# Optimization experiments

Hardware: AMD Instinct MI355X
Metric: run time of the kernel (lower is better)

The kernel has to match this reference:

```python
import jax, jax.numpy as jnp
import numpy as np

B_ = 2; L_ = 4096; D_MODEL = 1024; D_INNER = 2048; D_STATE = 128
N_HEADS = 32; HEADDIM = 64; D_CONV = 4; CHUNK = 64
CONV_DIM = D_INNER + 2 * D_STATE
EPS = 1e-5


def silu(x):
    return x * jax.nn.sigmoid(x)


def segsum(x):
    # x: (..., T) -> (..., T, T) stable segment sums; exp() gives 1-semiseparable matrix
    T = x.shape[-1]
    xe = jnp.broadcast_to(x[..., None], x.shape + (T,))  # (..., T, T)
    lower = jnp.tril(jnp.ones((T, T), bool), -1)
    xs = jnp.cumsum(jnp.where(lower, xe, 0.0), axis=-2)
    incl = jnp.tril(jnp.ones((T, T), bool), 0)
    return jnp.where(incl, xs, -jnp.inf)


def ssd(x, A, Bm, Cm):
    # x: (b, l, h, p); A: (b, l, h); Bm/Cm: (b, l, n) (single shared head, as in module)
    b, l, h, p = x.shape
    c = l // CHUNK
    x = x.reshape(b, c, CHUNK, h, p)
    A = A.reshape(b, c, CHUNK, h).transpose(0, 3, 1, 2)  # (b, h, c, l)
    Bm = Bm.reshape(b, c, CHUNK, D_STATE)
    Cm = Cm.reshape(b, c, CHUNK, D_STATE)
    A_cumsum = jnp.cumsum(A, axis=-1)                    # (b, h, c, l)
    Lmat = jnp.exp(segsum(A))                            # (b, h, c, l, l)
    # intra-chunk (diagonal blocks)
    Y_diag = jnp.einsum('bcln,bcsn,bhcls,bcshp->bclhp', Cm, Bm, Lmat, x)
    # per-chunk states
    decay_states = jnp.exp(A_cumsum[:, :, :, -1:] - A_cumsum)  # (b, h, c, l)
    states = jnp.einsum('bcln,bhcl,bclhp->bchpn', Bm, decay_states, x)
    init = jnp.zeros_like(states[:, :1])
    states = jnp.concatenate([init, states], axis=1)     # (b, c+1, h, p, n)
    A_last = jnp.pad(A_cumsum[:, :, :, -1], ((0, 0), (0, 0), (1, 0)))  # (b, h, c+1)
    decay_chunk = jnp.exp(segsum(A_last))                # (b, h, c+1, c+1)
    new_states = jnp.einsum('bhzc,bchpn->bzhpn', decay_chunk, states)
    states_prev = new_states[:, :-1]                     # (b, c, h, p, n)
    state_decay_out = jnp.exp(A_cumsum)
    Y_off = jnp.einsum('bcln,bchpn,bhcl->bclhp', Cm, states_prev, state_decay_out)
    return (Y_diag + Y_off).reshape(b, l, h, p)


def setup_inputs() -> dict:
    key = jax.random.key(0)
    ks = jax.random.split(key, 9)
    u = jax.random.normal(ks[0], (B_, L_, D_MODEL), jnp.float32)
    W_in = jax.random.normal(ks[1], (2 * D_INNER + 2 * D_STATE + N_HEADS, D_MODEL), jnp.float32) * (D_MODEL ** -0.5)
    conv_w = jax.random.normal(ks[2], (CONV_DIM, 1, D_CONV), jnp.float32) * 0.2
    conv_b = jax.random.normal(ks[3], (CONV_DIM,), jnp.float32) * 0.02
    dt_bias = jax.random.normal(ks[4], (N_HEADS,), jnp.float32) * 0.1
    A_log = jnp.log(jax.random.uniform(ks[5], (N_HEADS,), jnp.float32, 1.0, 16.0))
    D_param = jax.random.normal(ks[6], (N_HEADS,), jnp.float32) * 0.5
    norm_w = jnp.ones((D_INNER,), jnp.float32)
    W_out = jax.random.normal(ks[7], (D_MODEL, D_INNER), jnp.float32) * (D_INNER ** -0.5)
    return dict(u=u, W_in=W_in, conv_w=conv_w, conv_b=conv_b, dt_bias=dt_bias,
                A_log=A_log, D_param=D_param, norm_w=norm_w, W_out=W_out)


def mamba_forward(u, W_in, conv_w, conv_b, dt_bias, A_log, D_param, norm_w, W_out):
    b, l, _ = u.shape
    zxbcdt = u @ W_in.T                                  # (b, l, 2*di+2*ds+h)
    z = zxbcdt[..., :D_INNER]
    xBC = zxbcdt[..., D_INNER:D_INNER + CONV_DIM]
    dt = zxbcdt[..., D_INNER + CONV_DIM:]
    dt = jax.nn.softplus(dt + dt_bias)                   # (b, l, h)
    # causal depthwise conv1d
    xc = jnp.transpose(xBC, (0, 2, 1))                   # (b, conv_dim, l)
    xc = jax.lax.conv_general_dilated(xc, conv_w, (1,), [(D_CONV - 1, 0)],
                                      feature_group_count=CONV_DIM,
                                      dimension_numbers=('NCH', 'OIH', 'NCH'))
    xc = xc + conv_b[None, :, None]
    xBC = silu(jnp.transpose(xc, (0, 2, 1)))             # (b, l, conv_dim)
    x = xBC[..., :D_INNER]
    Bc = xBC[..., D_INNER:D_INNER + D_STATE]
    Cc = xBC[..., D_INNER + D_STATE:]
    x = x.reshape(b, l, N_HEADS, HEADDIM)
    A = -jnp.exp(A_log)                                  # (h,)
    Y = ssd(x * dt[..., None], A * dt, Bc, Cc)           # (b, l, h, p)
    y = Y + x * D_param[:, None]
    y = y.reshape(b, l, D_INNER)
    # gated RMSNorm
    y = y * silu(z)
    y = y * jax.lax.rsqrt(jnp.mean(y * y, axis=-1, keepdims=True) + EPS) * norm_w
    return y @ W_out.T


def reference(u, W_in, conv_w, conv_b, dt_bias, A_log, D_param, norm_w, W_out):
    return mamba_forward(u, W_in, conv_w, conv_b, dt_bias, A_log, D_param, norm_w, W_out)
```

## Files before the change

### kernel.cpp

```cpp
#include <hip/hip_runtime.h>
#include <hip/hip_bf16.h>
#include <math.h>

#define B_    2
#define L_    4096
#define DM    1024
#define DI    2048
#define DS    128
#define NH    32
#define HD    64
#define CHUNK 64
#define NC    (L_/CHUNK)
#define CD    (DI + 2*DS)
#define ROWS  (B_*L_)
#define NOUT  (2*DI + 2*DS + NH)
#define NPAD2 4608

typedef __attribute__((ext_vector_type(4))) float f32x4;
typedef __attribute__((ext_vector_type(8))) __bf16 bf16x8;
typedef __attribute__((ext_vector_type(4))) short s16x4;
typedef __attribute__((ext_vector_type(8))) short s16x8;

__global__ __launch_bounds__(256) void k_convert_all(const float* __restrict__ u, const float* __restrict__ W_in,
                                                     const float* __restrict__ W_out, __bf16* __restrict__ ubf,
                                                     __bf16* __restrict__ wibf, __bf16* __restrict__ wobf) {
    int i = blockIdx.x * 256 + threadIdx.x;
    const int QU  = ROWS * DM / 4;
    const int QWI = NPAD2 * DM / 4;
    const int QWO = DM * DI / 4;
    const float* s = nullptr;
    __bf16* d;
    bool zero = false;
    if (i < QU) {
        s = u + (size_t)i * 4; d = ubf + (size_t)i * 4;
    } else if (i < QU + QWI) {
        int j = i - QU;
        d = wibf + (size_t)j * 4;
        if (j < NOUT * DM / 4) s = W_in + (size_t)j * 4; else zero = true;
    } else if (i < QU + QWI + QWO) {
        int j = i - QU - QWI;
        s = W_out + (size_t)j * 4; d = wobf + (size_t)j * 4;
    } else return;
    s16x4 o = {0, 0, 0, 0};
    if (!zero) {
        f32x4 v = *(const f32x4*)s;
#pragma unroll
        for (int q = 0; q < 4; q++) o[q] = __builtin_bit_cast(short, (__bf16)v[q]);
    }
    *(s16x4*)d = o;
}

__device__ __forceinline__ void stage_half(const __bf16* __restrict__ G, int ldg, int grow0, int kt,
                                           char* lds, int ldsoff, int tid, int wave) {
#pragma unroll
    for (int issue = 0; issue < 2; issue++) {
        int o   = issue * 8192 + tid * 16;
        int row = o >> 7;
        int cb  = (o & 127) ^ ((row & 7) << 4);
        const __bf16* src = G + (size_t)(grow0 + row) * ldg + kt + (cb >> 1);
        char* ldsbase = lds + ldsoff + issue * 8192 + wave * 1024;
        __builtin_amdgcn_global_load_lds((const __attribute__((address_space(1))) void*)src,
                                         (__attribute__((address_space(3))) void*)ldsbase,
                                         16, 0, 0);
    }
}

__device__ __forceinline__ bf16x8 rdfrag(const char* lds, int ldsoff, int r, int ks, int lane) {
    int logical = r * 128 + ks * 64 + ((lane >> 4) << 4);
    int phys    = logical ^ ((r & 7) << 4);
    return *(const bf16x8*)(lds + ldsoff + phys);
}

__device__ __forceinline__ void gemm128x128_core(const __bf16* __restrict__ Ag, const __bf16* __restrict__ Bg,
                                                 int K, int m0, int n0, char* lds, f32x4 acc[4][2]) {
    const int tid = threadIdx.x, wave = tid >> 6, lane = tid & 63;
    const int wm = wave >> 2, wn = wave & 3, lrow = lane & 15;
    const int KT = K >> 6;

    for (int t = 0; t < KT; t++) {
        const int kt = t << 6;
        stage_half(Ag, K, m0, kt, lds, 0,     tid, wave);
        stage_half(Bg, K, n0, kt, lds, 16384, tid, wave);
        asm volatile("s_waitcnt vmcnt(0)" ::: "memory");
        __builtin_amdgcn_s_barrier();
        bf16x8 a[4][2];
#pragma unroll
        for (int fm = 0; fm < 4; fm++)
#pragma unroll
            for (int ks = 0; ks < 2; ks++)
                a[fm][ks] = rdfrag(lds, 0, wm * 64 + fm * 16 + lrow, ks, lane);
        __builtin_amdgcn_s_setprio(1);
#pragma unroll
        for (int fn = 0; fn < 2; fn++) {
            bf16x8 b0 = rdfrag(lds, 16384, wn * 32 + fn * 16 + lrow, 0, lane);
            bf16x8 b1 = rdfrag(lds, 16384, wn * 32 + fn * 16 + lrow, 1, lane);
#pragma unroll
            for (int fm = 0; fm < 4; fm++) {
                acc[fm][fn] = __builtin_amdgcn_mfma_f32_16x16x32_bf16(a[fm][0], b0, acc[fm][fn], 0, 0, 0);
                acc[fm][fn] = __builtin_amdgcn_mfma_f32_16x16x32_bf16(a[fm][1], b1, acc[fm][fn], 0, 0, 0);
            }
        }
        __builtin_amdgcn_s_setprio(0);
        __builtin_amdgcn_s_barrier();
    }
}

__global__ __launch_bounds__(512, 4) void k_gemm1(const __bf16* __restrict__ ubf, const __bf16* __restrict__ wibf,
                                                  __bf16* __restrict__ zbuf, __bf16* __restrict__ xbcraw,
                                                  float* __restrict__ dtbuf, const float* __restrict__ dt_bias) {
    extern __shared__ char lds[];
    f32x4 acc[4][2];
    f32x4 z4 = {0.f, 0.f, 0.f, 0.f};
#pragma unroll
    for (int i = 0; i < 4; i++)
#pragma unroll
        for (int j = 0; j < 2; j++) acc[i][j] = z4;

    int bid = blockIdx.x;
    int wg  = (bid & 7) * 280 + (bid >> 3);
    int m0  = (wg / 35) * 128;
    int n0  = (wg % 35) * 128;
    gemm128x128_core(ubf, wibf, DM, m0, n0, lds, acc);

    const int lane = threadIdx.x & 63, wave = threadIdx.x >> 6;
    const int wm = wave >> 2, wn = wave & 3;
    const int gm_base = m0 + wm * 64 + ((lane >> 4) << 2);
    const int gn_base = n0 + wn * 32 + (lane & 15);
#pragma unroll
    for (int fm = 0; fm < 4; fm++) {
        const int gmb = gm_base + fm * 16;
#pragma unroll
        for (int fn = 0; fn < 2; fn++) {
            const int gn = gn_base + fn * 16;
            if (gn < DI) {
#pragma unroll
                for (int r = 0; r < 4; r++)
                    zbuf[(size_t)(gmb + r) * DI + gn] = (__bf16)acc[fm][fn][r];
            } else if (gn < DI + CD) {
#pragma unroll
                for (int r = 0; r < 4; r++)
                    xbcraw[(size_t)(gmb + r) * CD + (gn - DI)] = (__bf16)acc[fm][fn][r];
            } else if (gn < NOUT) {
                const int hh = gn - (DI + CD);
                const float bb = dt_bias[hh];
#pragma unroll
                for (int r = 0; r < 4; r++) {
                    float x = acc[fm][fn][r] + bb;
                    float sp = (x > 20.f) ? x : log1pf(__expf(x));
                    dtbuf[(size_t)(gmb + r) * NH + hh] = sp;
                }
            }
        }
    }
}

__global__ __launch_bounds__(512, 4) void k_gemm2(const __bf16* __restrict__ ybf, const __bf16* __restrict__ wobf,
                                                  float* __restrict__ out) {
    extern __shared__ char lds[];
    f32x4 acc[4][2];
    f32x4 z4 = {0.f, 0.f, 0.f, 0.f};
#pragma unroll
    for (int i = 0; i < 4; i++)
#pragma unroll
        for (int j = 0; j < 2; j++) acc[i][j] = z4;

    int bid = blockIdx.x;
    int wg  = (bid & 7) * 64 + (bid >> 3);
    int m0  = (wg / 8) * 128;
    int n0  = (wg % 8) * 128;
    gemm128x128_core(ybf, wobf, DI, m0, n0, lds, acc);

    const int lane = threadIdx.x & 63, wave = threadIdx.x >> 6;
    const int wm = wave >> 2, wn = wave & 3;
    const int gm_base = m0 + wm * 64 + ((lane >> 4) << 2);
    const int gn_base = n0 + wn * 32 + (lane & 15);
#pragma unroll
    for (int fm = 0; fm < 4; fm++) {
        const int gmb = gm_base + fm * 16;
#pragma unroll
        for (int fn = 0; fn < 2; fn++) {
            const int gn = gn_base + fn * 16;
#pragma unroll
            for (int r = 0; r < 4; r++)
                out[(size_t)(gmb + r) * DM + gn] = acc[fm][fn][r];
        }
    }
}

__global__ __launch_bounds__(256) void k_conv(const __bf16* __restrict__ xbcraw, const float* __restrict__ conv_w,
                                              const float* __restrict__ conv_b, __bf16* __restrict__ xconv) {
    __shared__ float wsh[256 * 4];
    __shared__ float bsh[256];
    const int tid  = threadIdx.x;
    const int gsub = tid & 31;
    const int roct = tid >> 5;
    const int ch_base_blk = blockIdx.x * 256;
    *(f32x4*)&wsh[tid * 4] = *(const f32x4*)&conv_w[ch_base_blk * 4 + tid * 4];
    bsh[tid] = conv_b[ch_base_blk + tid];
    __syncthreads();

    const int ch0  = ch_base_blk + gsub * 8;
    const int row0 = (blockIdx.y * 8 + roct) * 8;
    const int l0   = row0 & (L_ - 1);
    const __bf16* src = xbcraw + (size_t)row0 * CD + ch0;

    s16x8 rr[11];
#pragma unroll
    for (int j = 0; j < 11; j++) {
        int ll = l0 - 3 + j;
        if (ll >= 0) rr[j] = *(const s16x8*)(src + (size_t)(j - 3) * CD);
        else         rr[j] = (s16x8){0, 0, 0, 0, 0, 0, 0, 0};
    }

    const int chl = gsub * 8;
    float w[8][4], bias[8];
#pragma unroll
    for (int j = 0; j < 8; j++) {
        bias[j] = bsh[chl + j];
#pragma unroll
        for (int k = 0; k < 4; k++) w[j][k] = wsh[(chl + j) * 4 + k];
    }

    __bf16* dst = xconv + (size_t)row0 * CD + ch0;
#pragma unroll
    for (int orow = 0; orow < 8; orow++) {
        float a[8];
#pragma unroll
        for (int j = 0; j < 8; j++) a[j] = bias[j];
#pragma unroll
        for (int k = 0; k < 4; k++) {
            s16x8 v = rr[orow + k];
#pragma unroll
            for (int j = 0; j < 8; j++)
                a[j] += w[j][k] * (float)__builtin_bit_cast(__bf16, (short)v[j]);
        }
        s16x8 o;
#pragma unroll
        for (int j = 0; j < 8; j++)
            o[j] = __builtin_bit_cast(short, (__bf16)(a[j] * __builtin_amdgcn_rcpf(1.f + __expf(-a[j]))));
        *(s16x8*)(dst + (size_t)orow * CD) = o;
    }
}

__global__ __launch_bounds__(256) void k_cbt(const __bf16* __restrict__ xconv, float* __restrict__ cbt) {
    const int c = blockIdx.x, b = blockIdx.y;
    const int tid = threadIdx.x, wv = tid >> 6, lane = tid & 63;
    const int lrow = lane & 15, lko = (lane >> 4) * 8;
    __shared__ __align__(16) __bf16 Csh[64 * 136];
    __shared__ __align__(16) __bf16 Bsh[64 * 136];
    const size_t rowbase = (size_t)b * L_ + c * CHUNK;
#pragma unroll
    for (int q = 0; q < 32; q++) {
        int i = q * 2 + (wv >> 1);
        int n = (wv & 1) * 64 + lane;
        const __bf16* base = xconv + (rowbase + i) * CD + DI;
        Bsh[i * 136 + n] = base[n];
        Csh[i * 136 + n] = base[DS + n];
    }
    __syncthreads();
    f32x4 acc[4];
    f32x4 z4 = {0.f, 0.f, 0.f, 0.f};
#pragma unroll
    for (int jt = 0; jt < 4; jt++) acc[jt] = z4;
#pragma unroll
    for (int ks = 0; ks < 4; ks++) {
        bf16x8 a = *(const bf16x8*)&Csh[(wv * 16 + lrow) * 136 + ks * 32 + lko];
#pragma unroll
        for (int jt = 0; jt < 4; jt++) {
            bf16x8 bb = *(const bf16x8*)&Bsh[(jt * 16 + lrow) * 136 + ks * 32 + lko];
            acc[jt] = __builtin_amdgcn_mfma_f32_16x16x32_bf16(a, bb, acc[jt], 0, 0, 0);
        }
    }
    float* o = cbt + (size_t)(b * NC + c) * 4096;
#pragma unroll
    for (int jt = 0; jt < 4; jt++)
#pragma unroll
        for (int r = 0; r < 4; r++) {
            int i = wv * 16 + (lane >> 4) * 4 + r;
            int j = jt * 16 + lrow;
            o[i * 64 + j] = acc[jt][r];
        }
}

__global__ __launch_bounds__(256) void k_ssd_a(const __bf16* __restrict__ xconv, const float* __restrict__ dtbuf,
                                               const float* __restrict__ cbt, const float* __restrict__ A_log,
                                               __bf16* __restrict__ ybuf, __bf16* __restrict__ states,
                                               float* __restrict__ asum, const float* __restrict__ D_param) {
    const int h = blockIdx.x, c = blockIdx.y, b = blockIdx.z;
    const int tid = threadIdx.x, wv = tid >> 6, lane = tid & 63;
    const int lrow = lane & 15, lko = (lane >> 4) * 8;
    __shared__ __align__(16) __bf16 xT[64 * 72];
    __shared__ __align__(16) __bf16 xsc[64 * 72];
    __shared__ __align__(16) __bf16 BT[128 * 72];
    __shared__ __align__(16) __bf16 Ms[64 * 72];
    __shared__ float dts[64], cum[64];

    const float Ah = -__expf(A_log[h]);
    const size_t rowbase = (size_t)b * L_ + c * CHUNK;

    float dtv = 0.f;
    if (wv == 0) { dtv = dtbuf[(rowbase + lane) * NH + h]; dts[lane] = dtv; }
#pragma unroll
    for (int q = 0; q < 16; q++) {
        int i = q * 4 + wv;
        xT[lane * 72 + i] = xconv[(rowbase + i) * CD + h * HD + lane];
    }
#pragma unroll
    for (int q = 0; q < 32; q++) {
        int i = q * 2 + (wv >> 1);
        int n = (wv & 1) * 64 + lane;
        BT[n * 72 + i] = xconv[(rowbase + i) * CD + DI + n];
    }
    if (wv == 0) {
        float v = Ah * dtv;
#pragma unroll
        for (int o = 1; o < 64; o <<= 1) { float t = __shfl_up(v, o); if (lane >= o) v += t; }
        cum[lane] = v;
        if (lane == 63) asum[(b * NC + c) * NH + h] = v;
    }
    __syncthreads();

    const float cum63 = cum[63];
    const float Dh = D_param[h];
    const float* cbt_bc = cbt + (size_t)(b * NC + c) * 4096;
#pragma unroll
    for (int q = 0; q < 16; q++) {
        int i = q * 4 + wv, j = lane;
        float cumi = cum[i];
        float m = 0.f;
        if (j <= i) m = cbt_bc[i * 64 + j] * __expf(cumi - cum[j]) * dts[j];
        if (j == i) m += Dh;
        Ms[i * 72 + j] = (__bf16)m;
        float dcfi = __expf(cum63 - cumi) * dts[i];
        xsc[lane * 72 + i] = (__bf16)((float)xT[lane * 72 + i] * dcfi);
    }
    __syncthreads();

    f32x4 z4 = {0.f, 0.f, 0.f, 0.f};
    {
        f32x4 accY[4];
#pragma unroll
        for (int pt = 0; pt < 4; pt++) accY[pt] = z4;
#pragma unroll
        for (int ks = 0; ks < 2; ks++) {
            bf16x8 a = *(const bf16x8*)&Ms[(wv * 16 + lrow) * 72 + ks * 32 + lko];
#pragma unroll
            for (int pt = 0; pt < 4; pt++) {
                bf16x8 bb = *(const bf16x8*)&xT[(pt * 16 + lrow) * 72 + ks * 32 + lko];
                accY[pt] = __builtin_amdgcn_mfma_f32_16x16x32_bf16(a, bb, accY[pt], 0, 0, 0);
            }
        }
#pragma unroll
        for (int pt = 0; pt < 4; pt++)
#pragma unroll
            for (int r = 0; r < 4; r++) {
                int i = wv * 16 + (lane >> 4) * 4 + r;
                int p = pt * 16 + lrow;
                ybuf[(rowbase + i) * DI + h * HD + p] = (__bf16)accY[pt][r];
            }
    }
    {
        f32x4 accS[8];
#pragma unroll
        for (int nt = 0; nt < 8; nt++) accS[nt] = z4;
#pragma unroll
        for (int ks = 0; ks < 2; ks++) {
            bf16x8 a = *(const bf16x8*)&xsc[(wv * 16 + lrow) * 72 + ks * 32 + lko];
#pragma unroll
            for (int nt = 0; nt < 8; nt++) {
                bf16x8 bb = *(const bf16x8*)&BT[(nt * 16 + lrow) * 72 + ks * 32 + lko];
                accS[nt] = __builtin_amdgcn_mfma_f32_16x16x32_bf16(a, bb, accS[nt], 0, 0, 0);
            }
        }
        __bf16* sp = states + ((size_t)(b * NC + c) * NH + h) * 8192;
#pragma unroll
        for (int nt = 0; nt < 8; nt++)
#pragma unroll
            for (int r = 0; r < 4; r++) {
                int p = wv * 16 + (lane >> 4) * 4 + r;
                int n = nt * 16 + lrow;
                sp[p * 128 + n] = (__bf16)accS[nt][r];
            }
    }
}

__global__ __launch_bounds__(256) void k_scan(__bf16* __restrict__ states, const float* __restrict__ asum) {
    const int seg = blockIdx.x, h = blockIdx.y, b = blockIdx.z;
    __shared__ float efs[NC];
    if (threadIdx.x < NC) efs[threadIdx.x] = __expf(asum[(b * NC + threadIdx.x) * NH + h]);
    __syncthreads();
    const int e0 = seg * 1024 + threadIdx.x * 4;
    __bf16* base = states + ((size_t)(b * NC) * NH + h) * 8192 + e0;
    const size_t cs = (size_t)NH * 8192;
    float S[4] = {0.f, 0.f, 0.f, 0.f};
    s16x4 r0 = *(const s16x4*)(base);
    s16x4 r1 = *(const s16x4*)(base + cs);
    s16x4 r2 = *(const s16x4*)(base + 2 * cs);
    s16x4 r3;
#define SCAN_STEP(RV, CC)                                                                  \
    {                                                                                      \
        s16x4 o; float e = efs[CC];                                                        \
        _Pragma("unroll")                                                                  \
        for (int q = 0; q < 4; q++) {                                                      \
            float t = (float)__builtin_bit_cast(__bf16, (short)RV[q]);                     \
            o[q] = __builtin_bit_cast(short, (__bf16)S[q]);                                \
            S[q] = e * S[q] + t;                                                           \
        }                                                                                  \
        *(s16x4*)(base + (size_t)(CC) * cs) = o;                                           \
    }
    for (int c = 0; c < NC; c += 4) {
        r3 = *(const s16x4*)(base + (size_t)(c + 3) * cs);
        SCAN_STEP(r0, c);
        if (c + 4 < NC) r0 = *(const s16x4*)(base + (size_t)(c + 4) * cs);
        SCAN_STEP(r1, c + 1);
        if (c + 5 < NC) r1 = *(const s16x4*)(base + (size_t)(c + 5) * cs);
        SCAN_STEP(r2, c + 2);
        if (c + 6 < NC) r2 = *(const s16x4*)(base + (size_t)(c + 6) * cs);
        SCAN_STEP(r3, c + 3);
    }
#undef SCAN_STEP
}

__global__ __launch_bounds__(256) void k_ssd_b(const __bf16* __restrict__ xconv, const float* __restrict__ dtbuf,
                                               const __bf16* __restrict__ states, const float* __restrict__ A_log,
                                               __bf16* __restrict__ ybuf) {
    const int h = blockIdx.x, c = blockIdx.y, b = blockIdx.z;
    const int tid = threadIdx.x, wv = tid >> 6, lane = tid & 63;
    const int lrow = lane & 15, lko = (lane >> 4) * 8;
    __shared__ __align__(16) __bf16 Csh[64 * 136];
    __shared__ __align__(16) __bf16 Sps[64 * 136];
    __shared__ float cum[64];

    const float Ah = -__expf(A_log[h]);
    const size_t rowbase = (size_t)b * L_ + c * CHUNK;
    const __bf16* sp = states + ((size_t)(b * NC + c) * NH + h) * 8192;
#pragma unroll
    for (int q = 0; q < 32; q++) {
        int i = q * 2 + (wv >> 1);
        int n = (wv & 1) * 64 + lane;
        Csh[i * 136 + n] = xconv[(rowbase + i) * CD + DI + DS + n];
        Sps[i * 136 + n] = sp[i * 128 + n];
    }
    if (wv == 0) {
        float v = Ah * dtbuf[(rowbase + lane) * NH + h];
#pragma unroll
        for (int o = 1; o < 64; o <<= 1) { float t = __shfl_up(v, o); if (lane >= o) v += t; }
        cum[lane] = v;
    }
    __syncthreads();

    f32x4 acc[4];
    f32x4 z4 = {0.f, 0.f, 0.f, 0.f};
#pragma unroll
    for (int pt = 0; pt < 4; pt++) acc[pt] = z4;
#pragma unroll
    for (int ks = 0; ks < 4; ks++) {
        bf16x8 a = *(const bf16x8*)&Csh[(wv * 16 + lrow) * 136 + ks * 32 + lko];
#pragma unroll
        for (int pt = 0; pt < 4; pt++) {
            bf16x8 bb = *(const bf16x8*)&Sps[(pt * 16 + lrow) * 136 + ks * 32 + lko];
            acc[pt] = __builtin_amdgcn_mfma_f32_16x16x32_bf16(a, bb, acc[pt], 0, 0, 0);
        }
    }
#pragma unroll
    for (int r = 0; r < 4; r++) {
        int i = wv * 16 + (lane >> 4) * 4 + r;
        float ef = __expf(cum[i]);
#pragma unroll
        for (int pt = 0; pt < 4; pt++) {
            size_t idx = (rowbase + i) * DI + h * HD + pt * 16 + lrow;
            float y0 = (float)ybuf[idx];
            ybuf[idx] = (__bf16)(y0 + ef * acc[pt][r]);
        }
    }
}

__global__ __launch_bounds__(256) void k_gate_norm(const __bf16* __restrict__ ybuf, const __bf16* __restrict__ zbuf,
                                                   const float* __restrict__ norm_w, __bf16* __restrict__ ybf) {
    const int r = blockIdx.x;
    const int tid = threadIdx.x;
    const int col0 = tid * 8;
    s16x8 y8 = *(const s16x8*)(ybuf + (size_t)r * DI + col0);
    s16x8 z8 = *(const s16x8*)(zbuf + (size_t)r * DI + col0);
    float v[8];
    float ss = 0.f;
#pragma unroll
    for (int q = 0; q < 8; q++) {
        float y = (float)__builtin_bit_cast(__bf16, (short)y8[q]);
        float z = (float)__builtin_bit_cast(__bf16, (short)z8[q]);
        float g = z * __builtin_amdgcn_rcpf(1.f + __expf(-z));
        v[q] = y * g;
        ss += v[q] * v[q];
    }
#pragma unroll
    for (int o = 32; o > 0; o >>= 1) ss += __shfl_down(ss, o);
    __shared__ float wsum[4];
    __shared__ float rmss;
    if ((tid & 63) == 0) wsum[tid >> 6] = ss;
    __syncthreads();
    if (tid == 0) {
        float t = wsum[0] + wsum[1] + wsum[2] + wsum[3];
        rmss = rsqrtf(t / (float)DI + 1e-5f);
    }
    __syncthreads();
    float rm = rmss;
    s16x8 o8;
#pragma unroll
    for (int q = 0; q < 8; q++)
        o8[q] = __builtin_bit_cast(short, (__bf16)(v[q] * rm * norm_w[col0 + q]));
    *(s16x8*)(ybf + (size_t)r * DI + col0) = o8;
}

extern "C" void kernel_launch(void* const* d_in, const int* in_sizes, int n_in,
                              void* d_out, int out_size, void* d_ws, size_t ws_size,
                              hipStream_t stream) {
    const float* u       = (const float*)d_in[0];
    const float* W_in    = (const float*)d_in[1];
    const float* conv_w  = (const float*)d_in[2];
    const float* conv_b  = (const float*)d_in[3];
    const float* dt_bias = (const float*)d_in[4];
    const float* A_log   = (const float*)d_in[5];
    const float* D_param = (const float*)d_in[6];
    const float* norm_w  = (const float*)d_in[7];
    const float* W_out   = (const float*)d_in[8];
    float* out = (float*)d_out;

    constexpr size_t OFF_WOBF  = 0;
    constexpr size_t OFF_ZBUF  = 4194304;
    constexpr size_t OFF_DT    = 37748736;
    constexpr size_t OFF_ASUM  = 38797312;
    constexpr size_t OFF_XCONV = 38813696;
    constexpr size_t OFF_CBT   = 76562432;
    constexpr size_t OFF_BIG   = 78659584;
    constexpr size_t NEED      = 145768448;
    if (ws_size < NEED) return;

    char* ws = (char*)d_ws;
    __bf16* wobf   = (__bf16*)(ws + OFF_WOBF);
    __bf16* zbuf   = (__bf16*)(ws + OFF_ZBUF);
    float*  dtbuf  = (float*) (ws + OFF_DT);
    float*  asum   = (float*) (ws + OFF_ASUM);
    __bf16* xconv  = (__bf16*)(ws + OFF_XCONV);
    float*  cbt    = (float*) (ws + OFF_CBT);
    __bf16* ubf    = (__bf16*)(ws + OFF_BIG);
    __bf16* wibf   = (__bf16*)(ws + OFF_BIG + 16777216);
    __bf16* xbcraw = (__bf16*)(ws + OFF_BIG + 16777216 + 9437184);
    __bf16* states = (__bf16*)(ws + OFF_BIG);
    __bf16* ybf    = (__bf16*)(ws + OFF_XCONV);
    __bf16* ybuf   = (__bf16*)d_out;

    (void)hipFuncSetAttribute((const void*)k_gemm1, hipFuncAttributeMaxDynamicSharedMemorySize, 32768);
    (void)hipFuncSetAttribute((const void*)k_gemm2, hipFuncAttributeMaxDynamicSharedMemorySize, 32768);

    constexpr int QTOT = ROWS * DM / 4 + NPAD2 * DM / 4 + DM * DI / 4;
    k_convert_all<<<(QTOT + 255) / 256, 256, 0, stream>>>(u, W_in, W_out, ubf, wibf, wobf);

    k_gemm1<<<2240, 512, 32768, stream>>>(ubf, wibf, zbuf, xbcraw, dtbuf, dt_bias);
    k_conv<<<dim3(9, 128), 256, 0, stream>>>(xbcraw, conv_w, conv_b, xconv);
    k_cbt<<<dim3(NC, B_), 256, 0, stream>>>(xconv, cbt);
    k_ssd_a<<<dim3(NH, NC, B_), 256, 0, stream>>>(xconv, dtbuf, cbt, A_log, ybuf, states, asum, D_param);
    k_scan<<<dim3(8, NH, B_), 256, 0, stream>>>(states, asum);
    k_ssd_b<<<dim3(NH, NC, B_), 256, 0, stream>>>(xconv, dtbuf, states, A_log, ybuf);
    k_gate_norm<<<ROWS, 256, 0, stream>>>(ybuf, zbuf, norm_w, ybf);
    k_gemm2<<<512, 512, 32768, stream>>>(ybf, wobf, out);
}
```

Before: 299.7 us.

## Move intra-chunk diagonal SSD output from ssd_a into ssd_b

The intra-chunk Y_diag computation (masked CB·decay matrix times x) moves out of the state kernel and into the off-diagonal kernel, which now sums both results in registers and writes ybuf once. This removes a bf16 write of Y_diag and its later read-modify-write, and drops one intermediate rounding. ssd_b now reloads x and cbt and uses more shared memory, which may lower its occupancy, while ssd_a becomes lighter.

```diff
diff --git a/kernel.cpp b/kernel.cpp
--- a/kernel.cpp
+++ b/kernel.cpp
@@ -283,16 +283,14 @@
 }
 
 __global__ __launch_bounds__(256) void k_ssd_a(const __bf16* __restrict__ xconv, const float* __restrict__ dtbuf,
-                                               const float* __restrict__ cbt, const float* __restrict__ A_log,
-                                               __bf16* __restrict__ ybuf, __bf16* __restrict__ states,
-                                               float* __restrict__ asum, const float* __restrict__ D_param) {
+                                               const float* __restrict__ A_log,
+                                               __bf16* __restrict__ states, float* __restrict__ asum) {
     const int h = blockIdx.x, c = blockIdx.y, b = blockIdx.z;
     const int tid = threadIdx.x, wv = tid >> 6, lane = tid & 63;
     const int lrow = lane & 15, lko = (lane >> 4) * 8;
     __shared__ __align__(16) __bf16 xT[64 * 72];
     __shared__ __align__(16) __bf16 xsc[64 * 72];
     __shared__ __align__(16) __bf16 BT[128 * 72];
-    __shared__ __align__(16) __bf16 Ms[64 * 72];
     __shared__ float dts[64], cum[64];
 
     const float Ah = -__expf(A_log[h]);
@@ -321,67 +319,36 @@
     __syncthreads();
 
     const float cum63 = cum[63];
-    const float Dh = D_param[h];
-    const float* cbt_bc = cbt + (size_t)(b * NC + c) * 4096;
 #pragma unroll
     for (int q = 0; q < 16; q++) {
-        int i = q * 4 + wv, j = lane;
-        float cumi = cum[i];
-        float m = 0.f;
-        if (j <= i) m = cbt_bc[i * 64 + j] * __expf(cumi - cum[j]) * dts[j];
-        if (j == i) m += Dh;
-        Ms[i * 72 + j] = (__bf16)m;
-        float dcfi = __expf(cum63 - cumi) * dts[i];
+        int i = q * 4 + wv;
+        float dcfi = __expf(cum63 - cum[i]) * dts[i];
         xsc[lane * 72 + i] = (__bf16)((float)xT[lane * 72 + i] * dcfi);
     }
     __syncthreads();
 
     f32x4 z4 = {0.f, 0.f, 0.f, 0.f};
-    {
-        f32x4 accY[4];
-#pragma unroll
-        for (int pt = 0; pt < 4; pt++) accY[pt] = z4;
-#pragma unroll
-        for (int ks = 0; ks < 2; ks++) {
-            bf16x8 a = *(const bf16x8*)&Ms[(wv * 16 + lrow) * 72 + ks * 32 + lko];
-#pragma unroll
-            for (int pt = 0; pt < 4; pt++) {
-                bf16x8 bb = *(const bf16x8*)&xT[(pt * 16 + lrow) * 72 + ks * 32 + lko];
-                accY[pt] = __builtin_amdgcn_mfma_f32_16x16x32_bf16(a, bb, accY[pt], 0, 0, 0);
-            }
-        }
-#pragma unroll
-        for (int pt = 0; pt < 4; pt++)
-#pragma unroll
-            for (int r = 0; r < 4; r++) {
-                int i = wv * 16 + (lane >> 4) * 4 + r;
-                int p = pt * 16 + lrow;
-                ybuf[(rowbase + i) * DI + h * HD + p] = (__bf16)accY[pt][r];
-            }
-    }
-    {
-        f32x4 accS[8];
-#pragma unroll
-        for (int nt = 0; nt < 8; nt++) accS[nt] = z4;
-#pragma unroll
-        for (int ks = 0; ks < 2; ks++) {
-            bf16x8 a = *(const bf16x8*)&xsc[(wv * 16 + lrow) * 72 + ks * 32 + lko];
-#pragma unroll
-            for (int nt = 0; nt < 8; nt++) {
-                bf16x8 bb = *(const bf16x8*)&BT[(nt * 16 + lrow) * 72 + ks * 32 + lko];
-                accS[nt] = __builtin_amdgcn_mfma_f32_16x16x32_bf16(a, bb, accS[nt], 0, 0, 0);
-            }
-        }
-        __bf16* sp = states + ((size_t)(b * NC + c) * NH + h) * 8192;
-#pragma unroll
-        for (int nt = 0; nt < 8; nt++)
-#pragma unroll
-            for (int r = 0; r < 4; r++) {
-                int p = wv * 16 + (lane >> 4) * 4 + r;
-                int n = nt * 16 + lrow;
-                sp[p * 128 + n] = (__bf16)accS[nt][r];
-            }
-    }
+    f32x4 accS[8];
+#pragma unroll
+    for (int nt = 0; nt < 8; nt++) accS[nt] = z4;
+#pragma unroll
+    for (int ks = 0; ks < 2; ks++) {
+        bf16x8 a = *(const bf16x8*)&xsc[(wv * 16 + lrow) * 72 + ks * 32 + lko];
+#pragma unroll
+        for (int nt = 0; nt < 8; nt++) {
+            bf16x8 bb = *(const bf16x8*)&BT[(nt * 16 + lrow) * 72 + ks * 32 + lko];
+            accS[nt] = __builtin_amdgcn_mfma_f32_16x16x32_bf16(a, bb, accS[nt], 0, 0, 0);
+        }
+    }
+    __bf16* sp = states + ((size_t)(b * NC + c) * NH + h) * 8192;
+#pragma unroll
+    for (int nt = 0; nt < 8; nt++)
+#pragma unroll
+        for (int r = 0; r < 4; r++) {
+            int p = wv * 16 + (lane >> 4) * 4 + r;
+            int n = nt * 16 + lrow;
+            sp[p * 128 + n] = (__bf16)accS[nt][r];
+        }
 }
 
 __global__ __launch_bounds__(256) void k_scan(__bf16* __restrict__ states, const float* __restrict__ asum) {
@@ -423,13 +390,16 @@
 
 __global__ __launch_bounds__(256) void k_ssd_b(const __bf16* __restrict__ xconv, const float* __restrict__ dtbuf,
                                                const __bf16* __restrict__ states, const float* __restrict__ A_log,
+                                               const float* __restrict__ cbt, const float* __restrict__ D_param,
                                                __bf16* __restrict__ ybuf) {
     const int h = blockIdx.x, c = blockIdx.y, b = blockIdx.z;
     const int tid = threadIdx.x, wv = tid >> 6, lane = tid & 63;
     const int lrow = lane & 15, lko = (lane >> 4) * 8;
+    __shared__ __align__(16) __bf16 xT[64 * 72];
+    __shared__ __align__(16) __bf16 Ms[64 * 72];
     __shared__ __align__(16) __bf16 Csh[64 * 136];
     __shared__ __align__(16) __bf16 Sps[64 * 136];
-    __shared__ float cum[64];
+    __shared__ float dts[64], cum[64];
 
     const float Ah = -__expf(A_log[h]);
     const size_t rowbase = (size_t)b * L_ + c * CHUNK;
@@ -441,25 +411,53 @@
         Csh[i * 136 + n] = xconv[(rowbase + i) * CD + DI + DS + n];
         Sps[i * 136 + n] = sp[i * 128 + n];
     }
+#pragma unroll
+    for (int q = 0; q < 16; q++) {
+        int i = q * 4 + wv;
+        xT[lane * 72 + i] = xconv[(rowbase + i) * CD + h * HD + lane];
+    }
     if (wv == 0) {
-        float v = Ah * dtbuf[(rowbase + lane) * NH + h];
+        float dtv = dtbuf[(rowbase + lane) * NH + h];
+        dts[lane] = dtv;
+        float v = Ah * dtv;
 #pragma unroll
         for (int o = 1; o < 64; o <<= 1) { float t = __shfl_up(v, o); if (lane >= o) v += t; }
         cum[lane] = v;
     }
     __syncthreads();
 
-    f32x4 acc[4];
+    const float Dh = D_param[h];
+    const float* cbt_bc = cbt + (size_t)(b * NC + c) * 4096;
+#pragma unroll
+    for (int q = 0; q < 16; q++) {
+        int i = q * 4 + wv, j = lane;
+        float m = 0.f;
+        if (j <= i) m = cbt_bc[i * 64 + j] * __expf(cum[i] - cum[j]) * dts[j];
+        if (j == i) m += Dh;
+        Ms[i * 72 + j] = (__bf16)m;
+    }
+    __syncthreads();
+
     f32x4 z4 = {0.f, 0.f, 0.f, 0.f};
-#pragma unroll
-    for (int pt = 0; pt < 4; pt++) acc[pt] = z4;
+    f32x4 accY[4], accO[4];
+#pragma unroll
+    for (int pt = 0; pt < 4; pt++) { accY[pt] = z4; accO[pt] = z4; }
+#pragma unroll
+    for (int ks = 0; ks < 2; ks++) {
+        bf16x8 a = *(const bf16x8*)&Ms[(wv * 16 + lrow) * 72 + ks * 32 + lko];
+#pragma unroll
+        for (int pt = 0; pt < 4; pt++) {
+            bf16x8 bb = *(const bf16x8*)&xT[(pt * 16 + lrow) * 72 + ks * 32 + lko];
+            accY[pt] = __builtin_amdgcn_mfma_f32_16x16x32_bf16(a, bb, accY[pt], 0, 0, 0);
+        }
+    }
 #pragma unroll
     for (int ks = 0; ks < 4; ks++) {
         bf16x8 a = *(const bf16x8*)&Csh[(wv * 16 + lrow) * 136 + ks * 32 + lko];
 #pragma unroll
         for (int pt = 0; pt < 4; pt++) {
             bf16x8 bb = *(const bf16x8*)&Sps[(pt * 16 + lrow) * 136 + ks * 32 + lko];
-            acc[pt] = __builtin_amdgcn_mfma_f32_16x16x32_bf16(a, bb, acc[pt], 0, 0, 0);
+            accO[pt] = __builtin_amdgcn_mfma_f32_16x16x32_bf16(a, bb, accO[pt], 0, 0, 0);
         }
     }
 #pragma unroll
@@ -469,8 +467,7 @@
 #pragma unroll
         for (int pt = 0; pt < 4; pt++) {
             size_t idx = (rowbase + i) * DI + h * HD + pt * 16 + lrow;
-            float y0 = (float)ybuf[idx];
-            ybuf[idx] = (__bf16)(y0 + ef * acc[pt][r]);
+            ybuf[idx] = (__bf16)(accY[pt][r] + ef * accO[pt][r]);
         }
     }
 }
@@ -558,9 +555,9 @@
     k_gemm1<<<2240, 512, 32768, stream>>>(ubf, wibf, zbuf, xbcraw, dtbuf, dt_bias);
     k_conv<<<dim3(9, 128), 256, 0, stream>>>(xbcraw, conv_w, conv_b, xconv);
     k_cbt<<<dim3(NC, B_), 256, 0, stream>>>(xconv, cbt);
-    k_ssd_a<<<dim3(NH, NC, B_), 256, 0, stream>>>(xconv, dtbuf, cbt, A_log, ybuf, states, asum, D_param);
+    k_ssd_a<<<dim3(NH, NC, B_), 256, 0, stream>>>(xconv, dtbuf, A_log, states, asum);
     k_scan<<<dim3(8, NH, B_), 256, 0, stream>>>(states, asum);
-    k_ssd_b<<<dim3(NH, NC, B_), 256, 0, stream>>>(xconv, dtbuf, states, A_log, ybuf);
+    k_ssd_b<<<dim3(NH, NC, B_), 256, 0, stream>>>(xconv, dtbuf, states, A_log, cbt, D_param, ybuf);
     k_gate_norm<<<ROWS, 256, 0, stream>>>(ybuf, zbuf, norm_w, ybf);
     k_gemm2<<<512, 512, 32768, stream>>>(ybf, wobf, out);
 }
```

Result: no change. 299.6 us, median of 2 (-0.0%).
